# Kernel optimization log

Hardware: AMD Instinct MI355X
Metric: run time of the kernel (lower is better)

Reference implementation:

```python
import jax, jax.numpy as jnp
import numpy as np

M = 64    # multiplicity (channels per harmonic degree)
P = 64    # positional encoding dim
EPS = 1e-5


def sinusoidal_pe(N, P):
    pos = jnp.arange(N, dtype=jnp.float32)[:, None]
    div = jnp.exp(jnp.arange(0, P, 2, dtype=jnp.float32) * (-np.log(10000.0) / P))
    pe = jnp.zeros((N, P), dtype=jnp.float32)
    pe = pe.at[:, 0::2].set(jnp.sin(pos * div))
    pe = pe.at[:, 1::2].set(jnp.cos(pos * div))
    return pe


def split_irreps(h):
    # h: [B, N, 4M] -> scalar part [B,N,M], vector part [B,N,M,3]
    B, N, _ = h.shape
    h4 = h.reshape(B, N, M, 4)
    return h4[..., 0], h4[..., 1:]


def merge_irreps(s, v):
    B, N, _ = s.shape
    return jnp.concatenate([s[..., None], v], axis=-1).reshape(B, N, M * 4)


def hyena_block(h, Wq, Wk, Wv, filt, Wo):
    # Hyena-style gated long convolution: q * conv(k * v), FFT circular conv along seq
    N = h.shape[1]
    q = h @ Wq
    k = h @ Wk
    v = h @ Wv
    kf = jnp.fft.rfft(filt, n=N, axis=0)                       # [N//2+1, H]
    conv = jnp.fft.irfft(jnp.fft.rfft(k * v, n=N, axis=1) * kf[None], n=N, axis=1)
    return (q * conv) @ Wo


def reg_linear(h, W0, W1):
    # degree-wise linear mixing across multiplicity (equivariant)
    s, v = split_irreps(h)
    return merge_irreps(jnp.einsum('bnm,mk->bnk', s, W0),
                        jnp.einsum('bnmd,mk->bnkd', v, W1))


def reg_batchnorm(h, g0, g1):
    # normalize per-channel irrep norms over (batch, tokens); learnable per-channel gain
    s, v = split_irreps(h)
    n0 = jnp.sqrt(jnp.mean(s * s, axis=(0, 1)) + EPS)          # [M]
    n1 = jnp.sqrt(jnp.mean(jnp.sum(v * v, axis=-1), axis=(0, 1)) + EPS)
    return merge_irreps(s / n0 * g0, v / n1[:, None] * g1[:, None])


def norm_activation(h):
    # norm-gated nonlinearity: each irrep scaled by sigmoid of its norm (equivariant)
    s, v = split_irreps(h)
    vn = jnp.sqrt(jnp.sum(v * v, axis=-1, keepdims=True) + EPS)
    return merge_irreps(s * jax.nn.sigmoid(jnp.abs(s)), v * jax.nn.sigmoid(vn))


def setup_inputs() -> dict:
    key = jax.random.key(0)
    B, N = 64, 1024
    D = M * 4
    H = [360, 360, 160]   # 10*sum(2l+1,l<=5)=360, 360, 10*sum(2l+1,l<=3)=160
    ks = iter(jax.random.split(key, 64))
    def rn(shape, scale=0.02):
        return jax.random.normal(next(ks), shape, dtype=jnp.float32) * scale
    inp = {
        'x': jax.random.normal(next(ks), (B, N, 3), dtype=jnp.float32),
        'tok_emb': rn((3, P)),
        'Wf': rn((P, M)),
        'wv': rn((M,), 0.5),
        'w_out': rn((M,), 0.5),
    }
    for i, Hi in enumerate(H, start=1):
        inp[f'Wq{i}'] = rn((D, Hi)); inp[f'Wk{i}'] = rn((D, Hi)); inp[f'Wv{i}'] = rn((D, Hi))
        inp[f'filt{i}'] = rn((N, Hi)); inp[f'Wo{i}'] = rn((Hi, D))
        inp[f'Wm0_{i}'] = rn((M, M)); inp[f'Wm1_{i}'] = rn((M, M))
        inp[f'g0_{i}'] = jnp.ones((M,), jnp.float32); inp[f'g1_{i}'] = jnp.ones((M,), jnp.float32)
    return inp


def reference(x, tok_emb, Wf, wv, w_out,
              Wq1, Wk1, Wv1, filt1, Wo1, Wm0_1, Wm1_1, g0_1, g1_1,
              Wq2, Wk2, Wv2, filt2, Wo2, Wm0_2, Wm1_2, g0_2, g1_2,
              Wq3, Wk3, Wv3, filt3, Wo3, Wm0_3, Wm1_3, g0_3, g1_3):
    B, N, _ = x.shape
    # invariant features: sinusoidal PE + token-type embedding (alternating 0/1, last token 2)
    pe = sinusoidal_pe(N, P)
    tt = jnp.arange(N) % 2
    tt = tt.at[-1].set(2)
    f = pe + tok_emb[tt]                                        # [N, P]
    # input conversion: invariants -> degree-0 channels; input vector -> degree-1 channels
    s0 = jnp.broadcast_to((f @ Wf)[None], (B, N, M))
    v0 = x[:, :, None, :] * wv[None, None, :, None]             # [B, N, M, 3]
    h = merge_irreps(s0, v0)                                    # [B, N, 4M]
    layers = [
        (Wq1, Wk1, Wv1, filt1, Wo1, Wm0_1, Wm1_1, g0_1, g1_1),
        (Wq2, Wk2, Wv2, filt2, Wo2, Wm0_2, Wm1_2, g0_2, g1_2),
        (Wq3, Wk3, Wv3, filt3, Wo3, Wm0_3, Wm1_3, g0_3, g1_3),
    ]
    for (Wq, Wk, Wv_, filt, Wo, Wm0, Wm1, g0, g1) in layers:
        h = h + hyena_block(h, Wq, Wk, Wv_, filt, Wo)           # hyena + residual
        y = reg_linear(h, Wm0, Wm1)                             # mlp
        y = reg_batchnorm(y, g0, g1)                            # batch norm
        y = norm_activation(y)                                  # norm activation
        h = h + y                                               # residual
    pooled = h.mean(axis=1)                                     # [B, 4M] mean pool over tokens
    _, vpool = split_irreps(pooled[:, None, :])                 # [B, 1, M, 3]
    return jnp.einsum('bmd,m->bd', vpool[:, 0], w_out)          # [B, 3]
```

## Files before the change

### kernel.cpp

```cpp
#include <hip/hip_runtime.h>
#include <math.h>

namespace {

typedef __bf16 bf16_t;
typedef bf16_t bf16x8 __attribute__((ext_vector_type(8)));
typedef float floatx4 __attribute__((ext_vector_type(4)));

constexpr int kN = 1024;
constexpr int kM = 64;
constexpr int kP = 64;
constexpr float kEps = 1e-5f;
constexpr int kFN = 1024;
constexpr size_t kYOFF = 16777216;

__device__ __forceinline__ float sigmoidf(float v) { return 1.0f / (1.0f + expf(-v)); }

__device__ __forceinline__ floatx4 mfma16(bf16x8 a, bf16x8 b, floatx4 c) {
  return __builtin_amdgcn_mfma_f32_16x16x32_bf16(a, b, c, 0, 0, 0);
}

__device__ __forceinline__ void fma3(floatx4& acc, bf16x8 ah, bf16x8 al,
                                     bf16x8 bh, bf16x8 bl) {
  acc = mfma16(ah, bh, acc);
  acc = mfma16(ah, bl, acc);
  acc = mfma16(al, bh, acc);
}

__device__ __forceinline__ void fma2(floatx4& acc, bf16x8 ah, bf16x8 bh, bf16x8 bl) {
  acc = mfma16(ah, bh, acc);
  acc = mfma16(ah, bl, acc);
}

union U4 { uint4 u; bf16_t b[8]; };
union Pk4 { uint2 u; bf16_t b[4]; };
union Ub2 { uint u; bf16_t b[2]; };

__device__ __forceinline__ void glds16(const bf16_t* g, bf16_t* l) {
  __builtin_amdgcn_global_load_lds(
      (const __attribute__((address_space(1))) void*)g,
      (__attribute__((address_space(3))) void*)l, 16, 0, 0);
}

__device__ __forceinline__ size_t hidx(int r, int d8) {
  const int rb = r >> 6, rr = r & 63;
  return (size_t)(rb * 8 + (d8 >> 2)) * 4096 + (rr >> 4) * 1024 + (d8 & 3) * 128 + (rr & 15) * 8;
}

__device__ __forceinline__ int zi(int i) { return i + (i >> 4); }

__device__ __forceinline__ float2 cadd(float2 a, float2 b) { return {a.x + b.x, a.y + b.y}; }
__device__ __forceinline__ float2 csub(float2 a, float2 b) { return {a.x - b.x, a.y - b.y}; }
__device__ __forceinline__ float2 cmul(float2 a, float2 w) {
  return {a.x * w.x - a.y * w.y, a.x * w.y + a.y * w.x};
}
__device__ __forceinline__ float2 cmulc(float2 a, float2 w) {
  return {a.x * w.x + a.y * w.y, a.y * w.x - a.x * w.y};
}

__global__ void k_s0(const float* __restrict__ tok_emb, const float* __restrict__ Wf,
                     float* __restrict__ s0) {
  __shared__ float f[kP];
  const int n = blockIdx.x;
  const int t = threadIdx.x;
  const int tt = (n == kN - 1) ? 2 : (n & 1);
  const int j = t >> 1;
  const float cexp = (float)(-9.210340371976184 / 64.0);
  const float divj = expf((float)(2 * j) * cexp);
  const float ang = (float)n * divj;
  const float pe = (t & 1) ? cosf(ang) : sinf(ang);
  f[t] = pe + tok_emb[tt * kP + t];
  __syncthreads();
  float acc = 0.0f;
#pragma unroll 8
  for (int p = 0; p < kP; ++p) acc = fmaf(f[p], Wf[p * kM + t], acc);
  s0[n * kM + t] = acc;
}

__global__ void k_h0(const float* __restrict__ x, const float* __restrict__ wv,
                     const float* __restrict__ s0, bf16_t* __restrict__ hsh) {
  const int idx = blockIdx.x * 256 + threadIdx.x;
  const int r = idx >> 5, d8 = idx & 31;
  const int n = r & (kN - 1);
  const int m0 = d8 * 2, m1 = m0 + 1;
  const float w0 = wv[m0], w1 = wv[m1];
  const float x0 = x[r * 3 + 0], x1 = x[r * 3 + 1], x2 = x[r * 3 + 2];
  float f[8];
  f[0] = s0[n * kM + m0]; f[1] = x0 * w0; f[2] = x1 * w0; f[3] = x2 * w0;
  f[4] = s0[n * kM + m1]; f[5] = x0 * w1; f[6] = x1 * w1; f[7] = x2 * w1;
  U4 oh, ol;
#pragma unroll
  for (int i = 0; i < 8; ++i) {
    const bf16_t h_ = (bf16_t)f[i];
    oh.b[i] = h_; ol.b[i] = (bf16_t)(f[i] - (float)h_);
  }
  const size_t base = hidx(r, d8);
  *(uint4*)(hsh + base) = oh.u;
  *(uint4*)(hsh + base + 512) = ol.u;
}

__global__ void k_wqkv3(const float* __restrict__ Wq0, const float* __restrict__ Wk0,
                        const float* __restrict__ Wv0,
                        const float* __restrict__ Wq1, const float* __restrict__ Wk1,
                        const float* __restrict__ Wv1,
                        const float* __restrict__ Wq2, const float* __restrict__ Wk2,
                        const float* __restrict__ Wv2, bf16_t* __restrict__ wall3) {
  const int l = blockIdx.y;
  const int H = (l == 2) ? 160 : 360;
  const int gy = (l == 2) ? 3 : 6;
  const int c = blockIdx.x;
  if (c >= gy * 64) return;
  const int k = threadIdx.x;
  const float* Wq = (l == 0) ? Wq0 : ((l == 1) ? Wq1 : Wq2);
  const float* Wk = (l == 0) ? Wk0 : ((l == 1) ? Wk1 : Wk2);
  const float* Wv = (l == 0) ? Wv0 : ((l == 1) ? Wv1 : Wv2);
  bf16_t* wall = wall3 + ((l == 2) ? 1179648 : (size_t)l * 589824);
  const bool ok = c < H;
  const float w[3] = {ok ? Wq[k * H + c] : 0.f, ok ? Wk[k * H + c] : 0.f,
                      ok ? Wv[k * H + c] : 0.f};
  const int ct = c >> 6, cgrp = (c >> 4) & 3, cl = c & 15;
  const int kc = k >> 5, quad = (k >> 3) & 3, off = k & 7;
  const size_t base = (size_t)(ct * 8 + kc) * 12288 + cgrp * 512 + quad * 128 + cl * 8 + off;
#pragma unroll
  for (int mat = 0; mat < 3; ++mat) {
    const bf16_t hi = (bf16_t)w[mat];
    wall[base + mat * 4096] = hi;
    wall[base + mat * 4096 + 2048] = (bf16_t)(w[mat] - (float)hi);
  }
}

__global__ void k_wo3(const float* __restrict__ Wo0, const float* __restrict__ Wo1,
                      const float* __restrict__ Wo2, bf16_t* __restrict__ WoF3) {
  const int l = blockIdx.y;
  const int H = (l == 2) ? 160 : 360;
  const float* Wo = (l == 0) ? Wo0 : ((l == 1) ? Wo1 : Wo2);
  bf16_t* WoF = WoF3 + (size_t)l * 196608;
  const int d = blockIdx.x;
  const int c = threadIdx.x;
  const float w = (c < H) ? Wo[c * 256 + d] : 0.f;
  const int dt = d >> 6, dgrp = (d >> 4) & 3, dl = d & 15;
  const int kc = c >> 5, quad = (c >> 3) & 3, off = c & 7;
  const size_t base = (size_t)(dt * 12 + kc) * 4096 + dgrp * 512 + quad * 128 + dl * 8 + off;
  const bf16_t hi = (bf16_t)w;
  WoF[base] = hi;
  WoF[base + 2048] = (bf16_t)(w - (float)hi);
}

__global__ void k_bt3(const float* __restrict__ W00, const float* __restrict__ W10,
                      const float* __restrict__ W01, const float* __restrict__ W11,
                      const float* __restrict__ W02, const float* __restrict__ W12,
                      bf16_t* __restrict__ BtF3) {
  const int l = blockIdx.y;
  const float* W0 = (l == 0) ? W00 : ((l == 1) ? W01 : W02);
  const float* W1 = (l == 0) ? W10 : ((l == 1) ? W11 : W12);
  bf16_t* BtF = BtF3 + (size_t)l * 131072;
  const int col = blockIdx.x, row = threadIdx.x;
  const int k = col >> 2, ck = col & 3, m = row >> 2, cm = row & 3;
  float v = 0.f;
  if (cm == ck) v = (ck == 0 ? W0 : W1)[m * 64 + k];
  const int ct = col >> 6, cgrp = (col >> 4) & 3, cl = col & 15;
  const int kc = row >> 5, quad = (row >> 3) & 3, off = row & 7;
  const size_t base = (size_t)(ct * 8 + kc) * 4096 + cgrp * 512 + quad * 128 + cl * 8 + off;
  const bf16_t hi = (bf16_t)v;
  BtF[base] = hi;
  BtF[base + 2048] = (bf16_t)(v - (float)hi);
}

__global__ void k_tw(float2* __restrict__ twg) {
  const int j = blockIdx.x * 256 + threadIdx.x;
  if (j < kFN / 2) {
    float s, c;
    sincosf(-6.283185307179586f * (float)j / (float)kFN, &s, &c);
    twg[j].x = c; twg[j].y = s;
  }
}

__device__ void fft_dif(float2* z, const float2* tw) {
  const int p = threadIdx.x;
#pragma unroll
  for (int m = 256; m >= 1; m >>= 2) {
    __syncthreads();
    const int pm = p & (m - 1);
    const int j = ((p & ~(m - 1)) << 2) | pm;
    const int tm2 = 512 / (2 * m), tm1 = 512 / m;
    const float2 x0 = z[zi(j)], x1 = z[zi(j + m)];
    const float2 x2 = z[zi(j + 2 * m)], x3 = z[zi(j + 3 * m)];
    const float2 w2 = tw[pm * tm2], w2b = tw[(pm + m) * tm2], w1 = tw[pm * tm1];
    const float2 a0 = cadd(x0, x2), a2 = cmul(csub(x0, x2), w2);
    const float2 a1 = cadd(x1, x3), a3 = cmul(csub(x1, x3), w2b);
    z[zi(j)]         = cadd(a0, a1);
    z[zi(j + m)]     = cmul(csub(a0, a1), w1);
    z[zi(j + 2 * m)] = cadd(a2, a3);
    z[zi(j + 3 * m)] = cmul(csub(a2, a3), w1);
  }
}

__device__ void fft_dit_inv(float2* z, const float2* tw) {
  const int p = threadIdx.x;
#pragma unroll
  for (int m = 1; m <= 256; m <<= 2) {
    __syncthreads();
    const int pm = p & (m - 1);
    const int j = ((p & ~(m - 1)) << 2) | pm;
    const int tm2 = 512 / (2 * m), tm1 = 512 / m;
    const float2 x0 = z[zi(j)], x1 = z[zi(j + m)];
    const float2 x2 = z[zi(j + 2 * m)], x3 = z[zi(j + 3 * m)];
    const float2 w1 = tw[pm * tm1], w2 = tw[pm * tm2], w2b = tw[(pm + m) * tm2];
    const float2 c1 = cmulc(x1, w1), c3 = cmulc(x3, w1);
    const float2 b0 = cadd(x0, c1), b1 = csub(x0, c1);
    const float2 b2 = cadd(x2, c3), b3 = csub(x2, c3);
    const float2 d2 = cmulc(b2, w2), d3 = cmulc(b3, w2b);
    z[zi(j)]         = cadd(b0, d2);
    z[zi(j + 2 * m)] = csub(b0, d2);
    z[zi(j + m)]     = cadd(b1, d3);
    z[zi(j + 3 * m)] = csub(b1, d3);
  }
}

__global__ __launch_bounds__(256) void k_kf3(const float* __restrict__ f0,
    const float* __restrict__ f1, const float* __restrict__ f2,
    const float2* __restrict__ twg, float2* __restrict__ kf3) {
  __shared__ float2 z[kFN + kFN / 16];
  __shared__ float2 tw[kFN / 2];
  const int bid = blockIdx.x;
  const int l = (bid < 360) ? 0 : ((bid < 720) ? 1 : 2);
  const int c = bid - ((l == 0) ? 0 : ((l == 1) ? 360 : 720));
  const int H = (l == 2) ? 160 : 360;
  const float* filt = (l == 0) ? f0 : ((l == 1) ? f1 : f2);
  float2* kf = kf3 + (size_t)l * 368640;
  for (int j = threadIdx.x; j < kFN / 2; j += 256) tw[j] = twg[j];
  for (int n = threadIdx.x; n < kFN; n += 256) {
    z[zi(n)].x = filt[n * H + c];
    z[zi(n)].y = 0.0f;
  }
  fft_dif(z, tw);
  __syncthreads();
  for (int j = threadIdx.x; j < kFN; j += 256) kf[c * kFN + j] = z[zi(j)];
}

__global__ __launch_bounds__(256) void k_conv(const bf16_t* __restrict__ kvb,
    const bf16_t* __restrict__ qb, bf16_t* __restrict__ prodb,
    const float2* __restrict__ kf, const float2* __restrict__ twg, int H) {
  __shared__ float2 z[kFN + kFN / 16];
  __shared__ float2 tw[kFN / 2];
  const int blk = blockIdx.x;
  const int c = blk % H;
  const int pb = blk / H;
  const size_t off0 = ((size_t)((2 * pb) * H + c)) << 10;
  const size_t off1 = ((size_t)((2 * pb + 1) * H + c)) << 10;
  for (int j = threadIdx.x; j < kFN / 2; j += 256) tw[j] = twg[j];
  for (int n2 = threadIdx.x; n2 < 512; n2 += 256) {
    Ub2 a0, a1;
    a0.u = *(const uint*)(kvb + off0 + 2 * n2);
    a1.u = *(const uint*)(kvb + off1 + 2 * n2);
    z[zi(2 * n2)].x = (float)a0.b[0];     z[zi(2 * n2)].y = (float)a1.b[0];
    z[zi(2 * n2 + 1)].x = (float)a0.b[1]; z[zi(2 * n2 + 1)].y = (float)a1.b[1];
  }
  fft_dif(z, tw);
  __syncthreads();
  for (int j = threadIdx.x; j < kFN; j += 256) {
    const float2 a = z[zi(j)];
    const float2 b = kf[c * kFN + j];
    float2 o;
    o.x = a.x * b.x - a.y * b.y;
    o.y = a.x * b.y + a.y * b.x;
    z[zi(j)] = o;
  }
  fft_dit_inv(z, tw);
  __syncthreads();
  const float s = 1.0f / (float)kFN;
  for (int n2 = threadIdx.x; n2 < 512; n2 += 256) {
    Ub2 q0, q1, o0, o1;
    q0.u = *(const uint*)(qb + off0 + 2 * n2);
    q1.u = *(const uint*)(qb + off1 + 2 * n2);
    o0.b[0] = (bf16_t)((z[zi(2 * n2)].x * s) * (float)q0.b[0]);
    o0.b[1] = (bf16_t)((z[zi(2 * n2 + 1)].x * s) * (float)q0.b[1]);
    o1.b[0] = (bf16_t)((z[zi(2 * n2)].y * s) * (float)q1.b[0]);
    o1.b[1] = (bf16_t)((z[zi(2 * n2 + 1)].y * s) * (float)q1.b[1]);
    *(uint*)(prodb + off0 + 2 * n2) = o0.u;
    *(uint*)(prodb + off1 + 2 * n2) = o1.u;
  }
}

__global__ __launch_bounds__(256) void k_qkv(const bf16_t* __restrict__ hsh,
    const bf16_t* __restrict__ wall, int H,
    bf16_t* __restrict__ qtb, bf16_t* __restrict__ kvb) {
  __shared__ bf16_t lds[20480];
  const int gy = (H + 63) >> 6;
  const int bid = blockIdx.x;
  const int xcd = bid & 7, sseq = bid >> 3;
  const int ct = sseq % gy;
  const int rb2 = (sseq / gy) * 8 + xcd;
  const int rb0 = rb2 * 2, rb1 = rb0 + 1;
  const int t = threadIdx.x;
  const int lane = t & 63, wave = t >> 6;
  const int l15 = lane & 15, quad = lane >> 4;
  const int c0 = ct * 64;
  const int wr = (wave & 1) * 32, wc = (wave >> 1) * 32;
  const int wr16 = (wave & 1) * 2, wc16 = (wave >> 1) * 2;
  const int q128l = quad * 128 + l15 * 8;
  floatx4 aq[2][2][2] = {}, ak_[2][2][2] = {}, av_[2][2][2] = {};
  for (int kt = 0; kt < 8; ++kt) {
    {
      const bf16_t* A0 = hsh + (size_t)(rb0 * 8 + kt) * 4096;
      const bf16_t* A1 = hsh + (size_t)(rb1 * 8 + kt) * 4096;
      const bf16_t* Bs = wall + (size_t)(ct * 8 + kt) * 12288;
#pragma unroll
      for (int s = 0; s < 10; ++s) {
        const int seg = wave * 10 + s;
        const bf16_t* src = (seg < 8) ? (A0 + seg * 512)
                          : (seg < 16) ? (A1 + (seg - 8) * 512)
                                       : (Bs + (seg - 16) * 512);
        glds16(src + lane * 8, &lds[seg * 512]);
      }
    }
    __syncthreads();
    bf16x8 ah[2][2], al[2][2];
#pragma unroll
    for (int rbx = 0; rbx < 2; ++rbx)
#pragma unroll
      for (int i = 0; i < 2; ++i) {
        ah[rbx][i] = *(const bf16x8*)(lds + rbx * 4096 + ((wr16 + i) * 2 + 0) * 512 + q128l);
        al[rbx][i] = *(const bf16x8*)(lds + rbx * 4096 + ((wr16 + i) * 2 + 1) * 512 + q128l);
      }
#pragma unroll
    for (int mat = 0; mat < 3; ++mat) {
      const int bb = 8192 + mat * 4096;
#pragma unroll
      for (int j = 0; j < 2; ++j) {
        const bf16x8 bh = *(const bf16x8*)(lds + bb + (wc16 + j) * 512 + q128l);
        const bf16x8 bl = *(const bf16x8*)(lds + bb + 2048 + (wc16 + j) * 512 + q128l);
#pragma unroll
        for (int rbx = 0; rbx < 2; ++rbx)
#pragma unroll
          for (int i = 0; i < 2; ++i) {
            floatx4& a = (mat == 0) ? aq[rbx][i][j]
                       : (mat == 1) ? ak_[rbx][i][j] : av_[rbx][i][j];
            fma3(a, ah[rbx][i], al[rbx][i], bh, bl);
          }
      }
    }
    __syncthreads();
  }
#pragma unroll
  for (int rbx = 0; rbx < 2; ++rbx) {
    const int r0 = (rb0 + rbx) * 64;
    const int b = r0 >> 10;
    const int n0 = r0 & 1023;
#pragma unroll
    for (int j = 0; j < 2; ++j) {
      const int c = c0 + wc + j * 16 + l15;
      if (c < H) {
        const size_t rbw = (((size_t)(b * H + c)) << 10) + n0 + wr + quad * 4;
#pragma unroll
        for (int i = 0; i < 2; ++i) {
          Pk4 pq, pk;
#pragma unroll
          for (int r = 0; r < 4; ++r) {
            pq.b[r] = (bf16_t)aq[rbx][i][j][r];
            pk.b[r] = (bf16_t)(ak_[rbx][i][j][r] * av_[rbx][i][j][r]);
          }
          *(uint2*)(qtb + rbw + i * 16) = pq.u;
          *(uint2*)(kvb + rbw + i * 16) = pk.u;
        }
      }
    }
  }
}

__global__ __launch_bounds__(256) void k_mix(const bf16_t* __restrict__ pv, int H, int KT,
    const bf16_t* __restrict__ WoF, bf16_t* __restrict__ hsh) {
  __shared__ float smem[4352];
  bf16_t* lsm = (bf16_t*)smem;
  const int r0 = blockIdx.x * 64;
  const int t = threadIdx.x;
  const int lane = t & 63, wave = t >> 6;
  const int l15 = lane & 15, quad = lane >> 4;
  const int b = r0 >> 10, n0 = r0 & 1023;
  const int wr = (wave & 1) * 32, wh = wave >> 1;
  const int q128l = quad * 128 + l15 * 8;
  floatx4 acc[2][8] = {};
  const int cl = t >> 3, n8 = (t & 7) * 8;
  for (int kt = 0; kt < KT; ++kt) {
    const int ck0 = kt * 32;
    __syncthreads();
    {
      const int c = ck0 + cl;
      U4 val;
      val.u = make_uint4(0, 0, 0, 0);
      if (c < H)
        val.u = *(const uint4*)(pv + ((((size_t)(b * H + c)) << 10) + n0 + n8));
#pragma unroll
      for (int u = 0; u < 8; ++u) lsm[(n8 + u) * 40 + cl] = val.b[u];
    }
    __syncthreads();
    const bf16x8 ah0 = *(const bf16x8*)(lsm + (wr + l15) * 40 + quad * 8);
    const bf16x8 ah1 = *(const bf16x8*)(lsm + (wr + 16 + l15) * 40 + quad * 8);
#pragma unroll
    for (int j = 0; j < 8; ++j) {
      const int jj = wh * 8 + j;
      const int dt = jj >> 2, dgrp = jj & 3;
      const bf16_t* Bb = WoF + (size_t)(dt * 12 + kt) * 4096 + dgrp * 512 + q128l;
      const bf16x8 bh = *(const bf16x8*)Bb;
      const bf16x8 bl = *(const bf16x8*)(Bb + 2048);
      fma2(acc[0][j], ah0, bh, bl);
      fma2(acc[1][j], ah1, bh, bl);
    }
  }
  const int nl = t >> 2, q4 = t & 3;
  const int r = r0 + nl;
#pragma unroll
  for (int g = 0; g < 4; ++g) {
    __syncthreads();
    if (wh == (g >> 1)) {
#pragma unroll
      for (int jl = 0; jl < 4; ++jl) {
        const int j = (g & 1) * 4 + jl;
#pragma unroll
        for (int i = 0; i < 2; ++i)
#pragma unroll
          for (int rr = 0; rr < 4; ++rr)
            smem[(wr + i * 16 + quad * 4 + rr) * 68 + jl * 16 + l15] = acc[i][j][rr];
      }
    }
    __syncthreads();
#pragma unroll
    for (int u8 = 0; u8 < 2; ++u8) {
      const int d8 = g * 8 + q4 * 2 + u8;
      const size_t base = hidx(r, d8);
      U4 hi, lo;
      hi.u = *(const uint4*)(hsh + base);
      lo.u = *(const uint4*)(hsh + base + 512);
      U4 oh, ol;
#pragma unroll
      for (int i = 0; i < 8; ++i) {
        const float f = (float)hi.b[i] + (float)lo.b[i] +
                        smem[nl * 68 + (q4 * 2 + u8) * 8 + i];
        const bf16_t h_ = (bf16_t)f;
        oh.b[i] = h_; ol.b[i] = (bf16_t)(f - (float)h_);
      }
      *(uint4*)(hsh + base) = oh.u;
      *(uint4*)(hsh + base + 512) = ol.u;
    }
  }
}

__global__ __launch_bounds__(256) void k_reg(const bf16_t* __restrict__ hsh,
    const bf16_t* __restrict__ BtF,
    bf16_t* __restrict__ ybf, float* __restrict__ partial) {
  __shared__ float smf[6144];
  __shared__ float red[256];
  bf16_t* lds = (bf16_t*)smf;
  const int bid = blockIdx.x;
  const int xcd = bid & 7, sseq = bid >> 3;
  const int ct = sseq & 3;
  const int rb2 = (sseq >> 2) * 8 + xcd;
  const int rb0 = rb2 * 2, rb1 = rb0 + 1;
  const int t = threadIdx.x;
  const int lane = t & 63, wave = t >> 6;
  const int l15 = lane & 15, quad = lane >> 4;
  const int c0 = ct * 64;
  const int wr = (wave & 1) * 32, wc = (wave >> 1) * 32;
  const int wr16 = (wave & 1) * 2, wc16 = (wave >> 1) * 2;
  const int q128l = quad * 128 + l15 * 8;
  floatx4 acc[2][2][2] = {};
  for (int kt = 0; kt < 8; ++kt) {
    {
      const bf16_t* A0 = hsh + (size_t)(rb0 * 8 + kt) * 4096;
      const bf16_t* A1 = hsh + (size_t)(rb1 * 8 + kt) * 4096;
      const bf16_t* Bs = BtF + (size_t)(ct * 8 + kt) * 4096;
#pragma unroll
      for (int s = 0; s < 6; ++s) {
        const int seg = wave * 6 + s;
        const bf16_t* src = (seg < 8) ? (A0 + seg * 512)
                          : (seg < 16) ? (A1 + (seg - 8) * 512)
                                       : (Bs + (seg - 16) * 512);
        glds16(src + lane * 8, &lds[seg * 512]);
      }
    }
    __syncthreads();
    bf16x8 ah[2][2], al[2][2];
#pragma unroll
    for (int rbx = 0; rbx < 2; ++rbx)
#pragma unroll
      for (int i = 0; i < 2; ++i) {
        ah[rbx][i] = *(const bf16x8*)(lds + rbx * 4096 + ((wr16 + i) * 2 + 0) * 512 + q128l);
        al[rbx][i] = *(const bf16x8*)(lds + rbx * 4096 + ((wr16 + i) * 2 + 1) * 512 + q128l);
      }
#pragma unroll
    for (int j = 0; j < 2; ++j) {
      const bf16x8 bh = *(const bf16x8*)(lds + 8192 + (wc16 + j) * 512 + q128l);
      const bf16x8 bl = *(const bf16x8*)(lds + 8192 + 2048 + (wc16 + j) * 512 + q128l);
#pragma unroll
      for (int rbx = 0; rbx < 2; ++rbx)
#pragma unroll
        for (int i = 0; i < 2; ++i)
          fma3(acc[rbx][i][j], ah[rbx][i], al[rbx][i], bh, bl);
    }
    __syncthreads();
  }
#pragma unroll
  for (int rbx = 0; rbx < 2; ++rbx)
#pragma unroll
    for (int j = 0; j < 2; ++j) {
      float s = 0.f;
#pragma unroll
      for (int i = 0; i < 2; ++i)
#pragma unroll
        for (int r = 0; r < 4; ++r)
          s = fmaf(acc[rbx][i][j][r], acc[rbx][i][j][r], s);
      s += __shfl_down(s, 32);
      s += __shfl_down(s, 16);
      if (lane < 16) red[rbx * 128 + wave * 32 + j * 16 + lane] = s;
    }
#pragma unroll
  for (int rbx = 0; rbx < 2; ++rbx) {
    __syncthreads();
#pragma unroll
    for (int i = 0; i < 2; ++i)
#pragma unroll
      for (int j = 0; j < 2; ++j)
#pragma unroll
        for (int r = 0; r < 4; ++r)
          smf[(wr + i * 16 + quad * 4 + r) * 68 + wc + j * 16 + l15] = acc[rbx][i][j][r];
    __syncthreads();
    const int nl = t >> 2, q4 = t & 3;
    const int r0 = (rb0 + rbx) * 64;
    const size_t gi = (size_t)(r0 + nl) * 256 + c0 + q4 * 16;
#pragma unroll
    for (int u2 = 0; u2 < 2; ++u2) {
      U4 oh, ol;
#pragma unroll
      for (int i = 0; i < 8; ++i) {
        const float f = smf[nl * 68 + q4 * 16 + u2 * 8 + i];
        const bf16_t h_ = (bf16_t)f;
        oh.b[i] = h_; ol.b[i] = (bf16_t)(f - (float)h_);
      }
      *(uint4*)(ybf + gi + u2 * 8) = oh.u;
      *(uint4*)(ybf + kYOFF + gi + u2 * 8) = ol.u;
    }
  }
  if (t < 64) {
    const int w0 = (t >= 32) ? 2 : 0;
    const float v0 = red[w0 * 32 + (t & 31)] + red[(w0 + 1) * 32 + (t & 31)];
    const float v1 = red[128 + w0 * 32 + (t & 31)] + red[128 + (w0 + 1) * 32 + (t & 31)];
    partial[(size_t)rb0 * 256 + c0 + t] = v0;
    partial[(size_t)rb1 * 256 + c0 + t] = v1;
  }
}

__global__ __launch_bounds__(256) void k_stat(const float* __restrict__ partial,
                                              float* __restrict__ st) {
  __shared__ float sm1[16][16];
  __shared__ float tot[16];
  const int bb = blockIdx.x;
  const int t = threadIdx.x;
  const int col16 = t & 15, rgrp = t >> 4;
  const int c = bb * 16 + col16;
  float s = 0.f;
  for (int r = rgrp; r < 1024; r += 16) s += partial[(size_t)r * 256 + c];
  sm1[rgrp][col16] = s;
  __syncthreads();
  if (t < 16) {
    float v = 0.f;
#pragma unroll
    for (int g = 0; g < 16; ++g) v += sm1[g][t];
    tot[t] = v;
  }
  __syncthreads();
  if (t < 4) {
    const int m = bb * 4 + t;
    st[m] = tot[4 * t];
    st[64 + m] = tot[4 * t + 1] + tot[4 * t + 2] + tot[4 * t + 3];
  }
}

__global__ void k_bnact(const bf16_t* __restrict__ ybf, const float* __restrict__ stats,
    const float* __restrict__ g0, const float* __restrict__ g1, bf16_t* __restrict__ hsh) {
  const int idx = blockIdx.x * 256 + threadIdx.x;
  const int r = idx >> 5, d8 = idx & 31;
  const int m0 = d8 * 2, m1 = m0 + 1;
  const float i00 = g0[m0] / sqrtf(stats[m0] * (1.0f / 65536.0f) + kEps);
  const float i10 = g1[m0] / sqrtf(stats[64 + m0] * (1.0f / 65536.0f) + kEps);
  const float i01 = g0[m1] / sqrtf(stats[m1] * (1.0f / 65536.0f) + kEps);
  const float i11 = g1[m1] / sqrtf(stats[64 + m1] * (1.0f / 65536.0f) + kEps);
  const size_t ye = (size_t)r * 256 + d8 * 8;
  U4 yh, yl;
  yh.u = *(const uint4*)(ybf + ye);
  yl.u = *(const uint4*)(ybf + kYOFF + ye);
  float yv[8];
#pragma unroll
  for (int i = 0; i < 8; ++i) yv[i] = (float)yh.b[i] + (float)yl.b[i];
  float a[8];
  {
    const float s = yv[0] * i00;
    const float vx = yv[1] * i10, vy = yv[2] * i10, vz = yv[3] * i10;
    const float so = s * sigmoidf(fabsf(s));
    const float vn = sqrtf(fmaf(vx, vx, fmaf(vy, vy, vz * vz)) + kEps);
    const float gv = sigmoidf(vn);
    a[0] = so; a[1] = vx * gv; a[2] = vy * gv; a[3] = vz * gv;
  }
  {
    const float s = yv[4] * i01;
    const float vx = yv[5] * i11, vy = yv[6] * i11, vz = yv[7] * i11;
    const float so = s * sigmoidf(fabsf(s));
    const float vn = sqrtf(fmaf(vx, vx, fmaf(vy, vy, vz * vz)) + kEps);
    const float gv = sigmoidf(vn);
    a[4] = so; a[5] = vx * gv; a[6] = vy * gv; a[7] = vz * gv;
  }
  const size_t base = hidx(r, d8);
  U4 hi, lo;
  hi.u = *(const uint4*)(hsh + base);
  lo.u = *(const uint4*)(hsh + base + 512);
  U4 oh, ol;
#pragma unroll
  for (int i = 0; i < 8; ++i) {
    const float f = (float)hi.b[i] + (float)lo.b[i] + a[i];
    const bf16_t h_ = (bf16_t)f;
    oh.b[i] = h_; ol.b[i] = (bf16_t)(f - (float)h_);
  }
  *(uint4*)(hsh + base) = oh.u;
  *(uint4*)(hsh + base + 512) = ol.u;
}

__global__ __launch_bounds__(256) void k_pool(const bf16_t* __restrict__ hsh,
    const float* __restrict__ w_out, float* __restrict__ out) {
  __shared__ float r0s[256], r1s[256], r2s[256];
  const int b = blockIdx.x;
  const int t = threadIdx.x;
  float p0 = 0, p1 = 0, p2 = 0;
  for (int idx = t; idx < kN * 32; idx += 256) {
    const int n = idx >> 5, d8 = idx & 31;
    const int r = (b << 10) + n;
    const size_t base = hidx(r, d8);
    U4 hi, lo;
    hi.u = *(const uint4*)(hsh + base);
    lo.u = *(const uint4*)(hsh + base + 512);
    const float w0 = w_out[d8 * 2], w1 = w_out[d8 * 2 + 1];
    p0 += ((float)hi.b[1] + (float)lo.b[1]) * w0 + ((float)hi.b[5] + (float)lo.b[5]) * w1;
    p1 += ((float)hi.b[2] + (float)lo.b[2]) * w0 + ((float)hi.b[6] + (float)lo.b[6]) * w1;
    p2 += ((float)hi.b[3] + (float)lo.b[3]) * w0 + ((float)hi.b[7] + (float)lo.b[7]) * w1;
  }
  r0s[t] = p0; r1s[t] = p1; r2s[t] = p2;
  __syncthreads();
  for (int s = 128; s > 0; s >>= 1) {
    if (t < s) { r0s[t] += r0s[t + s]; r1s[t] += r1s[t + s]; r2s[t] += r2s[t + s]; }
    __syncthreads();
  }
  if (t == 0) {
    out[b * 3 + 0] = r0s[0] * (1.0f / kN);
    out[b * 3 + 1] = r1s[0] * (1.0f / kN);
    out[b * 3 + 2] = r2s[0] * (1.0f / kN);
  }
}

}

extern "C" void kernel_launch(void* const* d_in, const int* in_sizes, int n_in,
                              void* d_out, int out_size, void* d_ws, size_t ws_size,
                              hipStream_t stream) {
  const float* x       = (const float*)d_in[0];
  const float* tok_emb = (const float*)d_in[1];
  const float* Wf      = (const float*)d_in[2];
  const float* wv      = (const float*)d_in[3];
  const float* w_out   = (const float*)d_in[4];

  float* ws    = (float*)d_ws;
  bf16_t* hsh  = (bf16_t*)ws;
  bf16_t* kvb  = (bf16_t*)(ws + 16777216);
  bf16_t* qtb  = (bf16_t*)(ws + 28573696);
  bf16_t* prodb = (bf16_t*)(ws + 40370176);
  bf16_t* ybf  = prodb;
  float*  partial = ws + 40370176 + 20000000;
  float*  s0   = ws + 40370176 + 23592960;
  float*  kf3  = s0 + 65536;
  bf16_t* wall3 = (bf16_t*)(kf3 + 1802240);
  bf16_t* WoF3  = wall3 + 1474560;
  bf16_t* BtF3  = WoF3 + 589824;
  float* stats = (float*)(BtF3 + 393216);
  float* twg   = stats + 384;

  k_tw<<<2, 256, 0, stream>>>((float2*)twg);
  k_s0<<<kN, 64, 0, stream>>>(tok_emb, Wf, s0);
  k_h0<<<8192, 256, 0, stream>>>(x, wv, s0, hsh);
  k_wqkv3<<<dim3(384, 3), 256, 0, stream>>>(
      (const float*)d_in[5], (const float*)d_in[6], (const float*)d_in[7],
      (const float*)d_in[14], (const float*)d_in[15], (const float*)d_in[16],
      (const float*)d_in[23], (const float*)d_in[24], (const float*)d_in[25], wall3);
  k_wo3<<<dim3(256, 3), 384, 0, stream>>>(
      (const float*)d_in[9], (const float*)d_in[18], (const float*)d_in[27], WoF3);
  k_bt3<<<dim3(256, 3), 256, 0, stream>>>(
      (const float*)d_in[10], (const float*)d_in[11],
      (const float*)d_in[19], (const float*)d_in[20],
      (const float*)d_in[28], (const float*)d_in[29], BtF3);
  k_kf3<<<880, 256, 0, stream>>>(
      (const float*)d_in[8], (const float*)d_in[17], (const float*)d_in[26],
      (const float2*)twg, (float2*)kf3);

  for (int l = 0; l < 3; ++l) {
    const float* g0   = (const float*)d_in[5 + 9 * l + 7];
    const float* g1   = (const float*)d_in[5 + 9 * l + 8];
    const int H = (l == 2) ? 160 : 360;
    const int gy = (H + 63) / 64;
    const int KT = gy * 2;
    bf16_t* wall = wall3 + ((l == 2) ? 1179648 : (size_t)l * 589824);
    bf16_t* WoF  = WoF3 + (size_t)l * 196608;
    bf16_t* BtF  = BtF3 + (size_t)l * 131072;
    const float2* kf = (const float2*)kf3 + (size_t)l * 368640;
    float* st = stats + l * 128;

    k_qkv<<<gy * 512, 256, 0, stream>>>(hsh, wall, H, qtb, kvb);
    k_conv<<<32 * H, 256, 0, stream>>>(kvb, qtb, prodb, kf, (const float2*)twg, H);
    k_mix<<<1024, 256, 0, stream>>>(prodb, H, KT, WoF, hsh);
    k_reg<<<2048, 256, 0, stream>>>(hsh, BtF, ybf, partial);
    k_stat<<<16, 256, 0, stream>>>(partial, st);
    k_bnact<<<8192, 256, 0, stream>>>(ybf, st, g0, g1, hsh);
  }

  k_pool<<<64, 256, 0, stream>>>(hsh, w_out, (float*)d_out);
}
```

Measured before the change: 1.193 ms.

## Double-buffer A tiles in LDS and load weight fragments directly from global

```diff
diff --git a/kernel.cpp b/kernel.cpp
--- a/kernel.cpp
+++ b/kernel.cpp
@@ -285,7 +285,7 @@
 __global__ __launch_bounds__(256) void k_qkv(const bf16_t* __restrict__ hsh,
     const bf16_t* __restrict__ wall, int H,
     bf16_t* __restrict__ qtb, bf16_t* __restrict__ kvb) {
-  __shared__ bf16_t lds[20480];
+  __shared__ bf16_t lds[16384];
   const int gy = (H + 63) >> 6;
   const int bid = blockIdx.x;
   const int xcd = bid & 7, sseq = bid >> 3;
@@ -300,36 +300,37 @@
   const int wr16 = (wave & 1) * 2, wc16 = (wave >> 1) * 2;
   const int q128l = quad * 128 + l15 * 8;
   floatx4 aq[2][2][2] = {}, ak_[2][2][2] = {}, av_[2][2][2] = {};
+  auto stageA = [&](int kt, int buf) {
+    const bf16_t* A0 = hsh + (size_t)(rb0 * 8 + kt) * 4096;
+    const bf16_t* A1 = hsh + (size_t)(rb1 * 8 + kt) * 4096;
+#pragma unroll
+    for (int s = 0; s < 4; ++s) {
+      const int seg = wave * 4 + s;
+      const bf16_t* src = (seg < 8) ? (A0 + seg * 512) : (A1 + (seg - 8) * 512);
+      glds16(src + lane * 8, &lds[buf * 8192 + seg * 512]);
+    }
+  };
+  stageA(0, 0);
+  __syncthreads();
   for (int kt = 0; kt < 8; ++kt) {
-    {
-      const bf16_t* A0 = hsh + (size_t)(rb0 * 8 + kt) * 4096;
-      const bf16_t* A1 = hsh + (size_t)(rb1 * 8 + kt) * 4096;
-      const bf16_t* Bs = wall + (size_t)(ct * 8 + kt) * 12288;
-#pragma unroll
-      for (int s = 0; s < 10; ++s) {
-        const int seg = wave * 10 + s;
-        const bf16_t* src = (seg < 8) ? (A0 + seg * 512)
-                          : (seg < 16) ? (A1 + (seg - 8) * 512)
-                                       : (Bs + (seg - 16) * 512);
-        glds16(src + lane * 8, &lds[seg * 512]);
+    const int cur = kt & 1;
+    if (kt < 7) stageA(kt + 1, cur ^ 1);
+    const bf16_t* Bk = wall + (size_t)(ct * 8 + kt) * 12288;
+    bf16x8 ah[2][2], al[2][2];
+#pragma unroll
+    for (int rbx = 0; rbx < 2; ++rbx)
+#pragma unroll
+      for (int i = 0; i < 2; ++i) {
+        ah[rbx][i] = *(const bf16x8*)(lds + cur * 8192 + rbx * 4096 + ((wr16 + i) * 2 + 0) * 512 + q128l);
+        al[rbx][i] = *(const bf16x8*)(lds + cur * 8192 + rbx * 4096 + ((wr16 + i) * 2 + 1) * 512 + q128l);
       }
-    }
-    __syncthreads();
-    bf16x8 ah[2][2], al[2][2];
-#pragma unroll
-    for (int rbx = 0; rbx < 2; ++rbx)
-#pragma unroll
-      for (int i = 0; i < 2; ++i) {
-        ah[rbx][i] = *(const bf16x8*)(lds + rbx * 4096 + ((wr16 + i) * 2 + 0) * 512 + q128l);
-        al[rbx][i] = *(const bf16x8*)(lds + rbx * 4096 + ((wr16 + i) * 2 + 1) * 512 + q128l);
-      }
 #pragma unroll
     for (int mat = 0; mat < 3; ++mat) {
-      const int bb = 8192 + mat * 4096;
 #pragma unroll
       for (int j = 0; j < 2; ++j) {
-        const bf16x8 bh = *(const bf16x8*)(lds + bb + (wc16 + j) * 512 + q128l);
-        const bf16x8 bl = *(const bf16x8*)(lds + bb + 2048 + (wc16 + j) * 512 + q128l);
+        const bf16_t* Bp = Bk + mat * 4096 + (wc16 + j) * 512 + q128l;
+        const bf16x8 bh = *(const bf16x8*)Bp;
+        const bf16x8 bl = *(const bf16x8*)(Bp + 2048);
 #pragma unroll
         for (int rbx = 0; rbx < 2; ++rbx)
 #pragma unroll
@@ -448,7 +449,7 @@
 __global__ __launch_bounds__(256) void k_reg(const bf16_t* __restrict__ hsh,
     const bf16_t* __restrict__ BtF,
     bf16_t* __restrict__ ybf, float* __restrict__ partial) {
-  __shared__ float smf[6144];
+  __shared__ float smf[8192];
   __shared__ float red[256];
   bf16_t* lds = (bf16_t*)smf;
   const int bid = blockIdx.x;
@@ -464,33 +465,34 @@
   const int wr16 = (wave & 1) * 2, wc16 = (wave >> 1) * 2;
   const int q128l = quad * 128 + l15 * 8;
   floatx4 acc[2][2][2] = {};
+  auto stageA = [&](int kt, int buf) {
+    const bf16_t* A0 = hsh + (size_t)(rb0 * 8 + kt) * 4096;
+    const bf16_t* A1 = hsh + (size_t)(rb1 * 8 + kt) * 4096;
+#pragma unroll
+    for (int s = 0; s < 4; ++s) {
+      const int seg = wave * 4 + s;
+      const bf16_t* src = (seg < 8) ? (A0 + seg * 512) : (A1 + (seg - 8) * 512);
+      glds16(src + lane * 8, &lds[buf * 8192 + seg * 512]);
+    }
+  };
+  stageA(0, 0);
+  __syncthreads();
   for (int kt = 0; kt < 8; ++kt) {
-    {
-      const bf16_t* A0 = hsh + (size_t)(rb0 * 8 + kt) * 4096;
-      const bf16_t* A1 = hsh + (size_t)(rb1 * 8 + kt) * 4096;
-      const bf16_t* Bs = BtF + (size_t)(ct * 8 + kt) * 4096;
-#pragma unroll
-      for (int s = 0; s < 6; ++s) {
-        const int seg = wave * 6 + s;
-        const bf16_t* src = (seg < 8) ? (A0 + seg * 512)
-                          : (seg < 16) ? (A1 + (seg - 8) * 512)
-                                       : (Bs + (seg - 16) * 512);
-        glds16(src + lane * 8, &lds[seg * 512]);
+    const int cur = kt & 1;
+    if (kt < 7) stageA(kt + 1, cur ^ 1);
+    bf16x8 ah[2][2], al[2][2];
+#pragma unroll
+    for (int rbx = 0; rbx < 2; ++rbx)
+#pragma unroll
+      for (int i = 0; i < 2; ++i) {
+        ah[rbx][i] = *(const bf16x8*)(lds + cur * 8192 + rbx * 4096 + ((wr16 + i) * 2 + 0) * 512 + q128l);
+        al[rbx][i] = *(const bf16x8*)(lds + cur * 8192 + rbx * 4096 + ((wr16 + i) * 2 + 1) * 512 + q128l);
       }
-    }
-    __syncthreads();
-    bf16x8 ah[2][2], al[2][2];
-#pragma unroll
-    for (int rbx = 0; rbx < 2; ++rbx)
-#pragma unroll
-      for (int i = 0; i < 2; ++i) {
-        ah[rbx][i] = *(const bf16x8*)(lds + rbx * 4096 + ((wr16 + i) * 2 + 0) * 512 + q128l);
-        al[rbx][i] = *(const bf16x8*)(lds + rbx * 4096 + ((wr16 + i) * 2 + 1) * 512 + q128l);
-      }
 #pragma unroll
     for (int j = 0; j < 2; ++j) {
-      const bf16x8 bh = *(const bf16x8*)(lds + 8192 + (wc16 + j) * 512 + q128l);
-      const bf16x8 bl = *(const bf16x8*)(lds + 8192 + 2048 + (wc16 + j) * 512 + q128l);
+      const bf16_t* Bp = BtF + (size_t)(ct * 8 + kt) * 4096 + (wc16 + j) * 512 + q128l;
+      const bf16x8 bh = *(const bf16x8*)Bp;
+      const bf16x8 bl = *(const bf16x8*)(Bp + 2048);
 #pragma unroll
       for (int rbx = 0; rbx < 2; ++rbx)
 #pragma unroll
```

Measured after the change: 1.211 ms. Within noise of the previous version (+1.5%).

## Double-buffer LDS staging in QKV and reg-linear GEMM kernels

Applied to the files above, without the earlier changes.

```diff
diff --git a/kernel.cpp b/kernel.cpp
--- a/kernel.cpp
+++ b/kernel.cpp
@@ -285,7 +285,7 @@
 __global__ __launch_bounds__(256) void k_qkv(const bf16_t* __restrict__ hsh,
     const bf16_t* __restrict__ wall, int H,
     bf16_t* __restrict__ qtb, bf16_t* __restrict__ kvb) {
-  __shared__ bf16_t lds[20480];
+  __shared__ bf16_t lds[40960];
   const int gy = (H + 63) >> 6;
   const int bid = blockIdx.x;
   const int xcd = bid & 7, sseq = bid >> 3;
@@ -300,36 +300,40 @@
   const int wr16 = (wave & 1) * 2, wc16 = (wave >> 1) * 2;
   const int q128l = quad * 128 + l15 * 8;
   floatx4 aq[2][2][2] = {}, ak_[2][2][2] = {}, av_[2][2][2] = {};
+  auto stage = [&](int kt, int buf) {
+    const bf16_t* A0 = hsh + (size_t)(rb0 * 8 + kt) * 4096;
+    const bf16_t* A1 = hsh + (size_t)(rb1 * 8 + kt) * 4096;
+    const bf16_t* Bs = wall + (size_t)(ct * 8 + kt) * 12288;
+#pragma unroll
+    for (int s = 0; s < 10; ++s) {
+      const int seg = wave * 10 + s;
+      const bf16_t* src = (seg < 8) ? (A0 + seg * 512)
+                        : (seg < 16) ? (A1 + (seg - 8) * 512)
+                                     : (Bs + (seg - 16) * 512);
+      glds16(src + lane * 8, &lds[buf * 20480 + seg * 512]);
+    }
+  };
+  stage(0, 0);
+  __syncthreads();
   for (int kt = 0; kt < 8; ++kt) {
-    {
-      const bf16_t* A0 = hsh + (size_t)(rb0 * 8 + kt) * 4096;
-      const bf16_t* A1 = hsh + (size_t)(rb1 * 8 + kt) * 4096;
-      const bf16_t* Bs = wall + (size_t)(ct * 8 + kt) * 12288;
-#pragma unroll
-      for (int s = 0; s < 10; ++s) {
-        const int seg = wave * 10 + s;
-        const bf16_t* src = (seg < 8) ? (A0 + seg * 512)
-                          : (seg < 16) ? (A1 + (seg - 8) * 512)
-                                       : (Bs + (seg - 16) * 512);
-        glds16(src + lane * 8, &lds[seg * 512]);
-      }
-    }
-    __syncthreads();
+    const int cur = kt & 1;
+    if (kt < 7) stage(kt + 1, cur ^ 1);
+    const bf16_t* Lb = lds + cur * 20480;
     bf16x8 ah[2][2], al[2][2];
 #pragma unroll
     for (int rbx = 0; rbx < 2; ++rbx)
 #pragma unroll
       for (int i = 0; i < 2; ++i) {
-        ah[rbx][i] = *(const bf16x8*)(lds + rbx * 4096 + ((wr16 + i) * 2 + 0) * 512 + q128l);
-        al[rbx][i] = *(const bf16x8*)(lds + rbx * 4096 + ((wr16 + i) * 2 + 1) * 512 + q128l);
+        ah[rbx][i] = *(const bf16x8*)(Lb + rbx * 4096 + ((wr16 + i) * 2 + 0) * 512 + q128l);
+        al[rbx][i] = *(const bf16x8*)(Lb + rbx * 4096 + ((wr16 + i) * 2 + 1) * 512 + q128l);
       }
 #pragma unroll
     for (int mat = 0; mat < 3; ++mat) {
       const int bb = 8192 + mat * 4096;
 #pragma unroll
       for (int j = 0; j < 2; ++j) {
-        const bf16x8 bh = *(const bf16x8*)(lds + bb + (wc16 + j) * 512 + q128l);
-        const bf16x8 bl = *(const bf16x8*)(lds + bb + 2048 + (wc16 + j) * 512 + q128l);
+        const bf16x8 bh = *(const bf16x8*)(Lb + bb + (wc16 + j) * 512 + q128l);
+        const bf16x8 bl = *(const bf16x8*)(Lb + bb + 2048 + (wc16 + j) * 512 + q128l);
 #pragma unroll
         for (int rbx = 0; rbx < 2; ++rbx)
 #pragma unroll
@@ -448,7 +452,7 @@
 __global__ __launch_bounds__(256) void k_reg(const bf16_t* __restrict__ hsh,
     const bf16_t* __restrict__ BtF,
     bf16_t* __restrict__ ybf, float* __restrict__ partial) {
-  __shared__ float smf[6144];
+  __shared__ float smf[12288];
   __shared__ float red[256];
   bf16_t* lds = (bf16_t*)smf;
   const int bid = blockIdx.x;
@@ -464,33 +468,37 @@
   const int wr16 = (wave & 1) * 2, wc16 = (wave >> 1) * 2;
   const int q128l = quad * 128 + l15 * 8;
   floatx4 acc[2][2][2] = {};
+  auto stage = [&](int kt, int buf) {
+    const bf16_t* A0 = hsh + (size_t)(rb0 * 8 + kt) * 4096;
+    const bf16_t* A1 = hsh + (size_t)(rb1 * 8 + kt) * 4096;
+    const bf16_t* Bs = BtF + (size_t)(ct * 8 + kt) * 4096;
+#pragma unroll
+    for (int s = 0; s < 6; ++s) {
+      const int seg = wave * 6 + s;
+      const bf16_t* src = (seg < 8) ? (A0 + seg * 512)
+                        : (seg < 16) ? (A1 + (seg - 8) * 512)
+                                     : (Bs + (seg - 16) * 512);
+      glds16(src + lane * 8, &lds[buf * 12288 + seg * 512]);
+    }
+  };
+  stage(0, 0);
+  __syncthreads();
   for (int kt = 0; kt < 8; ++kt) {
-    {
-      const bf16_t* A0 = hsh + (size_t)(rb0 * 8 + kt) * 4096;
-      const bf16_t* A1 = hsh + (size_t)(rb1 * 8 + kt) * 4096;
-      const bf16_t* Bs = BtF + (size_t)(ct * 8 + kt) * 4096;
-#pragma unroll
-      for (int s = 0; s < 6; ++s) {
-        const int seg = wave * 6 + s;
-        const bf16_t* src = (seg < 8) ? (A0 + seg * 512)
-                          : (seg < 16) ? (A1 + (seg - 8) * 512)
-                                       : (Bs + (seg - 16) * 512);
-        glds16(src + lane * 8, &lds[seg * 512]);
+    const int cur = kt & 1;
+    if (kt < 7) stage(kt + 1, cur ^ 1);
+    const bf16_t* Lb = lds + cur * 12288;
+    bf16x8 ah[2][2], al[2][2];
+#pragma unroll
+    for (int rbx = 0; rbx < 2; ++rbx)
+#pragma unroll
+      for (int i = 0; i < 2; ++i) {
+        ah[rbx][i] = *(const bf16x8*)(Lb + rbx * 4096 + ((wr16 + i) * 2 + 0) * 512 + q128l);
+        al[rbx][i] = *(const bf16x8*)(Lb + rbx * 4096 + ((wr16 + i) * 2 + 1) * 512 + q128l);
       }
-    }
-    __syncthreads();
-    bf16x8 ah[2][2], al[2][2];
-#pragma unroll
-    for (int rbx = 0; rbx < 2; ++rbx)
-#pragma unroll
-      for (int i = 0; i < 2; ++i) {
-        ah[rbx][i] = *(const bf16x8*)(lds + rbx * 4096 + ((wr16 + i) * 2 + 0) * 512 + q128l);
-        al[rbx][i] = *(const bf16x8*)(lds + rbx * 4096 + ((wr16 + i) * 2 + 1) * 512 + q128l);
-      }
 #pragma unroll
     for (int j = 0; j < 2; ++j) {
-      const bf16x8 bh = *(const bf16x8*)(lds + 8192 + (wc16 + j) * 512 + q128l);
-      const bf16x8 bl = *(const bf16x8*)(lds + 8192 + 2048 + (wc16 + j) * 512 + q128l);
+      const bf16x8 bh = *(const bf16x8*)(Lb + 8192 + (wc16 + j) * 512 + q128l);
+      const bf16x8 bl = *(const bf16x8*)(Lb + 8192 + 2048 + (wc16 + j) * 512 + q128l);
 #pragma unroll
       for (int rbx = 0; rbx < 2; ++rbx)
 #pragma unroll
```

Result: no change. 1.175 ms (-1.5%).

## Batch four sequences per FFT conv block and double-buffer k_reg LDS staging

Applied to the files above, without the earlier changes.

```diff
diff --git a/kernel.cpp b/kernel.cpp
--- a/kernel.cpp
+++ b/kernel.cpp
@@ -175,45 +175,64 @@
   }
 }
 
+__device__ __forceinline__ void dif_step(float2* z, const float2* tw, int m, int p) {
+  const int pm = p & (m - 1);
+  const int j = ((p & ~(m - 1)) << 2) | pm;
+  const int tm2 = 512 / (2 * m), tm1 = 512 / m;
+  const float2 x0 = z[zi(j)], x1 = z[zi(j + m)];
+  const float2 x2 = z[zi(j + 2 * m)], x3 = z[zi(j + 3 * m)];
+  const float2 w2 = tw[pm * tm2], w2b = tw[(pm + m) * tm2], w1 = tw[pm * tm1];
+  const float2 a0 = cadd(x0, x2), a2 = cmul(csub(x0, x2), w2);
+  const float2 a1 = cadd(x1, x3), a3 = cmul(csub(x1, x3), w2b);
+  z[zi(j)]         = cadd(a0, a1);
+  z[zi(j + m)]     = cmul(csub(a0, a1), w1);
+  z[zi(j + 2 * m)] = cadd(a2, a3);
+  z[zi(j + 3 * m)] = cmul(csub(a2, a3), w1);
+}
+
+__device__ __forceinline__ void dit_step(float2* z, const float2* tw, int m, int p) {
+  const int pm = p & (m - 1);
+  const int j = ((p & ~(m - 1)) << 2) | pm;
+  const int tm2 = 512 / (2 * m), tm1 = 512 / m;
+  const float2 x0 = z[zi(j)], x1 = z[zi(j + m)];
+  const float2 x2 = z[zi(j + 2 * m)], x3 = z[zi(j + 3 * m)];
+  const float2 w1 = tw[pm * tm1], w2 = tw[pm * tm2], w2b = tw[(pm + m) * tm2];
+  const float2 c1 = cmulc(x1, w1), c3 = cmulc(x3, w1);
+  const float2 b0 = cadd(x0, c1), b1 = csub(x0, c1);
+  const float2 b2 = cadd(x2, c3), b3 = csub(x2, c3);
+  const float2 d2 = cmulc(b2, w2), d3 = cmulc(b3, w2b);
+  z[zi(j)]         = cadd(b0, d2);
+  z[zi(j + 2 * m)] = csub(b0, d2);
+  z[zi(j + m)]     = cadd(b1, d3);
+  z[zi(j + 3 * m)] = csub(b1, d3);
+}
+
 __device__ void fft_dif(float2* z, const float2* tw) {
   const int p = threadIdx.x;
 #pragma unroll
   for (int m = 256; m >= 1; m >>= 2) {
     __syncthreads();
-    const int pm = p & (m - 1);
-    const int j = ((p & ~(m - 1)) << 2) | pm;
-    const int tm2 = 512 / (2 * m), tm1 = 512 / m;
-    const float2 x0 = z[zi(j)], x1 = z[zi(j + m)];
-    const float2 x2 = z[zi(j + 2 * m)], x3 = z[zi(j + 3 * m)];
-    const float2 w2 = tw[pm * tm2], w2b = tw[(pm + m) * tm2], w1 = tw[pm * tm1];
-    const float2 a0 = cadd(x0, x2), a2 = cmul(csub(x0, x2), w2);
-    const float2 a1 = cadd(x1, x3), a3 = cmul(csub(x1, x3), w2b);
-    z[zi(j)]         = cadd(a0, a1);
-    z[zi(j + m)]     = cmul(csub(a0, a1), w1);
-    z[zi(j + 2 * m)] = cadd(a2, a3);
-    z[zi(j + 3 * m)] = cmul(csub(a2, a3), w1);
-  }
-}
-
-__device__ void fft_dit_inv(float2* z, const float2* tw) {
+    dif_step(z, tw, m, p);
+  }
+}
+
+__device__ void fft_dif2(float2* za, float2* zb, const float2* tw) {
   const int p = threadIdx.x;
 #pragma unroll
+  for (int m = 256; m >= 1; m >>= 2) {
+    __syncthreads();
+    dif_step(za, tw, m, p);
+    dif_step(zb, tw, m, p);
+  }
+}
+
+__device__ void fft_dit_inv2(float2* za, float2* zb, const float2* tw) {
+  const int p = threadIdx.x;
+#pragma unroll
   for (int m = 1; m <= 256; m <<= 2) {
     __syncthreads();
-    const int pm = p & (m - 1);
-    const int j = ((p & ~(m - 1)) << 2) | pm;
-    const int tm2 = 512 / (2 * m), tm1 = 512 / m;
-    const float2 x0 = z[zi(j)], x1 = z[zi(j + m)];
-    const float2 x2 = z[zi(j + 2 * m)], x3 = z[zi(j + 3 * m)];
-    const float2 w1 = tw[pm * tm1], w2 = tw[pm * tm2], w2b = tw[(pm + m) * tm2];
-    const float2 c1 = cmulc(x1, w1), c3 = cmulc(x3, w1);
-    const float2 b0 = cadd(x0, c1), b1 = csub(x0, c1);
-    const float2 b2 = cadd(x2, c3), b3 = csub(x2, c3);
-    const float2 d2 = cmulc(b2, w2), d3 = cmulc(b3, w2b);
-    z[zi(j)]         = cadd(b0, d2);
-    z[zi(j + 2 * m)] = csub(b0, d2);
-    z[zi(j + m)]     = cadd(b1, d3);
-    z[zi(j + 3 * m)] = csub(b1, d3);
+    dit_step(za, tw, m, p);
+    dit_step(zb, tw, m, p);
   }
 }
 
@@ -241,44 +260,64 @@
 __global__ __launch_bounds__(256) void k_conv(const bf16_t* __restrict__ kvb,
     const bf16_t* __restrict__ qb, bf16_t* __restrict__ prodb,
     const float2* __restrict__ kf, const float2* __restrict__ twg, int H) {
-  __shared__ float2 z[kFN + kFN / 16];
+  __shared__ float2 za[kFN + kFN / 16];
+  __shared__ float2 zb[kFN + kFN / 16];
   __shared__ float2 tw[kFN / 2];
   const int blk = blockIdx.x;
   const int c = blk % H;
   const int pb = blk / H;
-  const size_t off0 = ((size_t)((2 * pb) * H + c)) << 10;
-  const size_t off1 = ((size_t)((2 * pb + 1) * H + c)) << 10;
+  const size_t off0 = ((size_t)((4 * pb) * H + c)) << 10;
+  const size_t off1 = ((size_t)((4 * pb + 1) * H + c)) << 10;
+  const size_t off2 = ((size_t)((4 * pb + 2) * H + c)) << 10;
+  const size_t off3 = ((size_t)((4 * pb + 3) * H + c)) << 10;
   for (int j = threadIdx.x; j < kFN / 2; j += 256) tw[j] = twg[j];
   for (int n2 = threadIdx.x; n2 < 512; n2 += 256) {
-    Ub2 a0, a1;
+    Ub2 a0, a1, a2, a3;
     a0.u = *(const uint*)(kvb + off0 + 2 * n2);
     a1.u = *(const uint*)(kvb + off1 + 2 * n2);
-    z[zi(2 * n2)].x = (float)a0.b[0];     z[zi(2 * n2)].y = (float)a1.b[0];
-    z[zi(2 * n2 + 1)].x = (float)a0.b[1]; z[zi(2 * n2 + 1)].y = (float)a1.b[1];
-  }
-  fft_dif(z, tw);
+    a2.u = *(const uint*)(kvb + off2 + 2 * n2);
+    a3.u = *(const uint*)(kvb + off3 + 2 * n2);
+    za[zi(2 * n2)].x = (float)a0.b[0];     za[zi(2 * n2)].y = (float)a1.b[0];
+    za[zi(2 * n2 + 1)].x = (float)a0.b[1]; za[zi(2 * n2 + 1)].y = (float)a1.b[1];
+    zb[zi(2 * n2)].x = (float)a2.b[0];     zb[zi(2 * n2)].y = (float)a3.b[0];
+    zb[zi(2 * n2 + 1)].x = (float)a2.b[1]; zb[zi(2 * n2 + 1)].y = (float)a3.b[1];
+  }
+  fft_dif2(za, zb, tw);
   __syncthreads();
   for (int j = threadIdx.x; j < kFN; j += 256) {
-    const float2 a = z[zi(j)];
     const float2 b = kf[c * kFN + j];
+    const float2 a = za[zi(j)];
     float2 o;
     o.x = a.x * b.x - a.y * b.y;
     o.y = a.x * b.y + a.y * b.x;
-    z[zi(j)] = o;
-  }
-  fft_dit_inv(z, tw);
+    za[zi(j)] = o;
+    const float2 a2_ = zb[zi(j)];
+    float2 o2;
+    o2.x = a2_.x * b.x - a2_.y * b.y;
+    o2.y = a2_.x * b.y + a2_.y * b.x;
+    zb[zi(j)] = o2;
+  }
+  fft_dit_inv2(za, zb, tw);
   __syncthreads();
   const float s = 1.0f / (float)kFN;
   for (int n2 = threadIdx.x; n2 < 512; n2 += 256) {
-    Ub2 q0, q1, o0, o1;
+    Ub2 q0, q1, q2, q3, o0, o1, o2, o3;
     q0.u = *(const uint*)(qb + off0 + 2 * n2);
     q1.u = *(const uint*)(qb + off1 + 2 * n2);
-    o0.b[0] = (bf16_t)((z[zi(2 * n2)].x * s) * (float)q0.b[0]);
-    o0.b[1] = (bf16_t)((z[zi(2 * n2 + 1)].x * s) * (float)q0.b[1]);
-    o1.b[0] = (bf16_t)((z[zi(2 * n2)].y * s) * (float)q1.b[0]);
-    o1.b[1] = (bf16_t)((z[zi(2 * n2 + 1)].y * s) * (float)q1.b[1]);
+    q2.u = *(const uint*)(qb + off2 + 2 * n2);
+    q3.u = *(const uint*)(qb + off3 + 2 * n2);
+    o0.b[0] = (bf16_t)((za[zi(2 * n2)].x * s) * (float)q0.b[0]);
+    o0.b[1] = (bf16_t)((za[zi(2 * n2 + 1)].x * s) * (float)q0.b[1]);
+    o1.b[0] = (bf16_t)((za[zi(2 * n2)].y * s) * (float)q1.b[0]);
+    o1.b[1] = (bf16_t)((za[zi(2 * n2 + 1)].y * s) * (float)q1.b[1]);
+    o2.b[0] = (bf16_t)((zb[zi(2 * n2)].x * s) * (float)q2.b[0]);
+    o2.b[1] = (bf16_t)((zb[zi(2 * n2 + 1)].x * s) * (float)q2.b[1]);
+    o3.b[0] = (bf16_t)((zb[zi(2 * n2)].y * s) * (float)q3.b[0]);
+    o3.b[1] = (bf16_t)((zb[zi(2 * n2 + 1)].y * s) * (float)q3.b[1]);
     *(uint*)(prodb + off0 + 2 * n2) = o0.u;
     *(uint*)(prodb + off1 + 2 * n2) = o1.u;
+    *(uint*)(prodb + off2 + 2 * n2) = o2.u;
+    *(uint*)(prodb + off3 + 2 * n2) = o3.u;
   }
 }
 
@@ -448,7 +487,7 @@
 __global__ __launch_bounds__(256) void k_reg(const bf16_t* __restrict__ hsh,
     const bf16_t* __restrict__ BtF,
     bf16_t* __restrict__ ybf, float* __restrict__ partial) {
-  __shared__ float smf[6144];
+  __shared__ float smf[12288];
   __shared__ float red[256];
   bf16_t* lds = (bf16_t*)smf;
   const int bid = blockIdx.x;
@@ -464,33 +503,37 @@
   const int wr16 = (wave & 1) * 2, wc16 = (wave >> 1) * 2;
   const int q128l = quad * 128 + l15 * 8;
   floatx4 acc[2][2][2] = {};
+  auto stage = [&](int kt, int buf) {
+    const bf16_t* A0 = hsh + (size_t)(rb0 * 8 + kt) * 4096;
+    const bf16_t* A1 = hsh + (size_t)(rb1 * 8 + kt) * 4096;
+    const bf16_t* Bs = BtF + (size_t)(ct * 8 + kt) * 4096;
+#pragma unroll
+    for (int s = 0; s < 6; ++s) {
+      const int seg = wave * 6 + s;
+      const bf16_t* src = (seg < 8) ? (A0 + seg * 512)
+                        : (seg < 16) ? (A1 + (seg - 8) * 512)
+                                     : (Bs + (seg - 16) * 512);
+      glds16(src + lane * 8, &lds[buf * 12288 + seg * 512]);
+    }
+  };
+  stage(0, 0);
+  __syncthreads();
   for (int kt = 0; kt < 8; ++kt) {
-    {
-      const bf16_t* A0 = hsh + (size_t)(rb0 * 8 + kt) * 4096;
-      const bf16_t* A1 = hsh + (size_t)(rb1 * 8 + kt) * 4096;
-      const bf16_t* Bs = BtF + (size_t)(ct * 8 + kt) * 4096;
-#pragma unroll
-      for (int s = 0; s < 6; ++s) {
-        const int seg = wave * 6 + s;
-        const bf16_t* src = (seg < 8) ? (A0 + seg * 512)
-                          : (seg < 16) ? (A1 + (seg - 8) * 512)
-                                       : (Bs + (seg - 16) * 512);
-        glds16(src + lane * 8, &lds[seg * 512]);
+    const int cur = kt & 1;
+    if (kt < 7) stage(kt + 1, cur ^ 1);
+    const bf16_t* Lb = lds + cur * 12288;
+    bf16x8 ah[2][2], al[2][2];
+#pragma unroll
+    for (int rbx = 0; rbx < 2; ++rbx)
+#pragma unroll
+      for (int i = 0; i < 2; ++i) {
+        ah[rbx][i] = *(const bf16x8*)(Lb + rbx * 4096 + ((wr16 + i) * 2 + 0) * 512 + q128l);
+        al[rbx][i] = *(const bf16x8*)(Lb + rbx * 4096 + ((wr16 + i) * 2 + 1) * 512 + q128l);
       }
-    }
-    __syncthreads();
-    bf16x8 ah[2][2], al[2][2];
-#pragma unroll
-    for (int rbx = 0; rbx < 2; ++rbx)
-#pragma unroll
-      for (int i = 0; i < 2; ++i) {
-        ah[rbx][i] = *(const bf16x8*)(lds + rbx * 4096 + ((wr16 + i) * 2 + 0) * 512 + q128l);
-        al[rbx][i] = *(const bf16x8*)(lds + rbx * 4096 + ((wr16 + i) * 2 + 1) * 512 + q128l);
-      }
 #pragma unroll
     for (int j = 0; j < 2; ++j) {
-      const bf16x8 bh = *(const bf16x8*)(lds + 8192 + (wc16 + j) * 512 + q128l);
-      const bf16x8 bl = *(const bf16x8*)(lds + 8192 + 2048 + (wc16 + j) * 512 + q128l);
+      const bf16x8 bh = *(const bf16x8*)(Lb + 8192 + (wc16 + j) * 512 + q128l);
+      const bf16x8 bl = *(const bf16x8*)(Lb + 8192 + 2048 + (wc16 + j) * 512 + q128l);
 #pragma unroll
       for (int rbx = 0; rbx < 2; ++rbx)
 #pragma unroll
@@ -710,7 +753,7 @@
     float* st = stats + l * 128;
 
     k_qkv<<<gy * 512, 256, 0, stream>>>(hsh, wall, H, qtb, kvb);
-    k_conv<<<32 * H, 256, 0, stream>>>(kvb, qtb, prodb, kf, (const float2*)twg, H);
+    k_conv<<<16 * H, 256, 0, stream>>>(kvb, qtb, prodb, kf, (const float2*)twg, H);
     k_mix<<<1024, 256, 0, stream>>>(prodb, H, KT, WoF, hsh);
     k_reg<<<2048, 256, 0, stream>>>(hsh, BtF, ybf, partial);
     k_stat<<<16, 256, 0, stream>>>(partial, st);
```

Result: faster. 1.146 ms (-4.0%).
